# Kernel tuning notes

Measured on AMD Instinct MI355X. Metric: run time of the kernel, lower is better.

Reference implementation:

```python
import jax, jax.numpy as jnp
import numpy as np

N, E, H = 25000, 100000, 32          # nodes, edges, node/clique hidden dim
NC, A, EC = 8000, 50000, 24000       # cliques, node2clique assignments, clique edges
EEMB, CEE, L = 8, 8, 2               # edge emb dims, n layers


def segment_mean(vals, ids, num):
    s = jax.ops.segment_sum(vals, ids, num_segments=num)
    cnt = jax.ops.segment_sum(jnp.ones(ids.shape[0], vals.dtype), ids, num_segments=num)
    return s / jnp.maximum(cnt, 1.0)[:, None]


def setup_inputs() -> dict:
    key = jax.random.key(0)
    ks = jax.random.split(key, 24)
    s = 0.1  # param scale
    inp = {
        "node_features": jax.random.normal(ks[0], (N, H), jnp.float32),
        "edge_index": jax.random.randint(ks[1], (2, E), 0, N),
        "edge_features": jax.random.normal(ks[2], (E, EEMB), jnp.float32),
        "clique_features": jax.random.normal(ks[3], (NC, H), jnp.float32),
        "node2clique_index": jnp.stack([
            jax.random.randint(ks[4], (A,), 0, N),
            jax.random.randint(ks[5], (A,), 0, NC)]),
        "clique_edge_index": jax.random.randint(ks[6], (2, EC), 0, NC),
        "clique_edge_features": jax.random.normal(ks[7], (EC, CEE), jnp.float32),
        # node NNConv params (stacked over L layers)
        "nn1_w": jax.random.normal(ks[8], (L, EEMB, H)) * s,
        "nn1_b": jnp.zeros((L, H)),
        "nn2_w": jax.random.normal(ks[9], (L, H, H * H)) * s,
        "nn2_b": jnp.zeros((L, H * H)),
        "root_w": jax.random.normal(ks[10], (L, H, H)) * s,
        "root_b": jnp.zeros((L, H)),
        # Node2Clique linear
        "n2c_w": jax.random.normal(ks[11], (L, H, H)) * s,
        "n2c_b": jnp.zeros((L, H)),
        # clique NNConv params
        "cnn1_w": jax.random.normal(ks[12], (L, CEE, H)) * s,
        "cnn1_b": jnp.zeros((L, H)),
        "cnn2_w": jax.random.normal(ks[13], (L, H, H * H)) * s,
        "cnn2_b": jnp.zeros((L, H * H)),
        "croot_w": jax.random.normal(ks[14], (L, H, H)) * s,
        "croot_b": jnp.zeros((L, H)),
        # Clique2Node linear
        "c2n_w": jax.random.normal(ks[15], (L, H, H)) * s,
        "c2n_b": jnp.zeros((L, H)),
    }
    return inp


def nnconv(x, src, dst, edge_attr, w1, b1, w2, b2, rw, rb, n_out_nodes):
    # per-edge weight matrices from the edge MLP: [E, in, out]
    h = jax.nn.relu(edge_attr @ w1 + b1)
    We = (h @ w2 + b2).reshape(edge_attr.shape[0], x.shape[1], -1)
    msg = jnp.einsum('ei,eio->eo', x[src], We)           # message from source
    agg = segment_mean(msg, dst, n_out_nodes)            # mean aggregation at target
    return agg + x @ rw + rb                             # root weight + bias


def reference(node_features, edge_index, edge_features, clique_features,
              node2clique_index, clique_edge_index, clique_edge_features,
              nn1_w, nn1_b, nn2_w, nn2_b, root_w, root_b, n2c_w, n2c_b,
              cnn1_w, cnn1_b, cnn2_w, cnn2_b, croot_w, croot_b, c2n_w, c2n_b):
    x, c = node_features, clique_features
    src, dst = edge_index[0], edge_index[1]
    nid, cid = node2clique_index[0], node2clique_index[1]
    csrc, cdst = clique_edge_index[0], clique_edge_index[1]
    for l in range(L):
        # node-level edge-conditioned conv
        x = jax.nn.relu(nnconv(x, src, dst, edge_features,
                               nn1_w[l], nn1_b[l], nn2_w[l], nn2_b[l],
                               root_w[l], root_b[l], N))
        # Node2Clique: project node feats, scatter-mean into cliques
        m = x @ n2c_w[l] + n2c_b[l]
        c = c + segment_mean(m[nid], cid, NC)
        # clique-level edge-conditioned conv
        c = jax.nn.relu(nnconv(c, csrc, cdst, clique_edge_features,
                               cnn1_w[l], cnn1_b[l], cnn2_w[l], cnn2_b[l],
                               croot_w[l], croot_b[l], NC))
        # Clique2Node: project clique feats, scatter-mean back onto nodes
        m = c @ c2n_w[l] + c2n_b[l]
        x = x + segment_mean(m[cid], nid, N)
    return (x, c)
```

## Files before the change

### kernel.cpp

```cpp
#include <hip/hip_runtime.h>
#include <hip/hip_bf16.h>

typedef unsigned int u32;
typedef unsigned short u16;

#define DEVINL __device__ __forceinline__

constexpr int Nn  = 25000;
constexpr int Ee  = 100000;
constexpr int NCc = 8000;
constexpr int Aa  = 50000;
constexpr int ECc = 24000;
constexpr int TCOLS = 1088;
constexpr int WPSZ  = TCOLS*32;
constexpr int TSP   = 1064;
constexpr int NB_N = (Nn + 255)/256;
constexpr int NB_C = (NCc + 255)/256;

typedef float f32x4 __attribute__((ext_vector_type(4)));
typedef short s16x8 __attribute__((ext_vector_type(8)));

DEVINL float b2f(u16 u){ union{u32 i;float f;}v; v.i = ((u32)u)<<16; return v.f; }
DEVINL float bfl(u32 u){ union{u32 i;float f;}v; v.i = u<<16; return v.f; }
DEVINL float bfh(u32 u){ union{u32 i;float f;}v; v.i = u & 0xffff0000u; return v.f; }
DEVINL u16 f2b(float f){ union{float f;u32 i;}v; v.f=f; u32 i=v.i;
  return (u16)((i + 0x7fffu + ((i>>16)&1u)) >> 16); }
DEVINL u32 pk2(float a, float b){ return (u32)f2b(a) | ((u32)f2b(b) << 16); }
DEVINL float ldw(const void* p, long i, int f){
  return f ? ((const float*)p)[i] : b2f(((const u16*)p)[i]);
}

__global__ __launch_bounds__(256) void k_detect(const u16* __restrict__ p, int n,
                        u32* __restrict__ maxbits, int* __restrict__ zcnt,
                        int* __restrict__ done, int* __restrict__ flag){
  int i0 = blockIdx.x*256 + threadIdx.x;
  float lm = 0.f; int lz = 0;
  for (int i = i0; i < n; i += gridDim.x*256){
    u16 v = p[i];
    if (v == 0) lz++;
    lm = fmaxf(lm, fabsf(b2f(v)));
  }
  #pragma unroll
  for (int off = 32; off; off >>= 1){
    lm = fmaxf(lm, __shfl_down(lm, off));
    lz += __shfl_down(lz, off);
  }
  if ((threadIdx.x & 63) == 0){
    atomicMax(maxbits, __float_as_uint(lm));
    atomicAdd(zcnt, lz);
  }
  __syncthreads();
  if (threadIdx.x == 0){
    __threadfence();
    if (atomicAdd(done, 1) == gridDim.x - 1){
      float m = __uint_as_float(*maxbits);
      *flag = (m > 1e6f || *zcnt > n/4) ? 1 : 0;
    }
  }
}

__global__ __launch_bounds__(256) void k_count_all(const int* __restrict__ ei, const int* __restrict__ cei,
                          const int* __restrict__ n2c,
                          int* __restrict__ deg_nd, int* __restrict__ deg_ce,
                          int* __restrict__ deg_n2c, int* __restrict__ deg_c2n,
                          int* __restrict__ cnt_sn, int* __restrict__ cnt_sc){
  int i = blockIdx.x*256 + threadIdx.x;
  if (i < Ee)                             atomicAdd(&deg_nd[ei[Ee + i]], 1);
  else if ((i -= Ee) < ECc)               atomicAdd(&deg_ce[cei[ECc + i]], 1);
  else if ((i -= ECc) < Aa)               atomicAdd(&deg_n2c[n2c[Aa + i]], 1);
  else if ((i -= Aa) < Aa)                atomicAdd(&deg_c2n[n2c[i]], 1);
  else if ((i -= Aa) < Ee)                atomicAdd(&cnt_sn[ei[i]], 1);
  else if ((i -= Ee) < ECc)               atomicAdd(&cnt_sc[cei[i]], 1);
}

__global__ __launch_bounds__(256) void k_scan_block(
    const int* __restrict__ c0, const int* __restrict__ c1,
    const int* __restrict__ c2, const int* __restrict__ c3,
    int* __restrict__ o0, int* __restrict__ o1, int* __restrict__ o2, int* __restrict__ o3,
    int* __restrict__ b0, int* __restrict__ b1, int* __restrict__ b2, int* __restrict__ b3){
  __shared__ int s[256];
  int bid = blockIdx.x, seg, rb;
  if (bid < NB_N){ seg=0; rb=bid; }
  else if (bid < NB_N+NB_C){ seg=1; rb=bid-NB_N; }
  else if (bid < 2*NB_N+NB_C){ seg=2; rb=bid-NB_N-NB_C; }
  else { seg=3; rb=bid-2*NB_N-NB_C; }
  const int* cnt = seg==0?c0 : seg==1?c1 : seg==2?c2 : c3;
  int* offs = seg==0?o0 : seg==1?o1 : seg==2?o2 : o3;
  int* bs   = seg==0?b0 : seg==1?b1 : seg==2?b2 : b3;
  int M = (seg & 1) ? NCc : Nn;
  int tid = threadIdx.x;
  int i = rb*256 + tid;
  int v = (i < M) ? cnt[i] : 0;
  s[tid] = v; __syncthreads();
  for (int d = 1; d < 256; d <<= 1){
    int t = (tid >= d) ? s[tid-d] : 0;
    __syncthreads();
    s[tid] += t;
    __syncthreads();
  }
  if (i < M) offs[i] = s[tid] - v;
  if (tid == 255) bs[rb] = s[255];
}

__global__ __launch_bounds__(512) void k_spine(int* __restrict__ b0, int* __restrict__ b1,
                      int* __restrict__ b2, int* __restrict__ b3){
  __shared__ int s[512];
  int tid = threadIdx.x, seg = tid >> 7, lane = tid & 127;
  int NB = (seg & 1) ? NB_C : NB_N;
  int* bp = seg==0?b0 : seg==1?b1 : seg==2?b2 : b3;
  int v = (lane < NB) ? bp[lane] : 0;
  s[tid] = v; __syncthreads();
  for (int d = 1; d < 128; d <<= 1){
    int t = (lane >= d) ? s[tid-d] : 0;
    __syncthreads();
    s[tid] += t;
    __syncthreads();
  }
  if (lane < NB) bp[lane] = s[tid] - v;
}

__global__ __launch_bounds__(256) void k_scan_fix(
    int* __restrict__ o0, int* __restrict__ o1, int* __restrict__ o2, int* __restrict__ o3,
    const int* __restrict__ b0, const int* __restrict__ b1,
    const int* __restrict__ b2, const int* __restrict__ b3){
  int i = blockIdx.x*256 + threadIdx.x;
  if (i < Nn) o0[i] += b0[i >> 8];
  else if ((i -= Nn) < NCc) o1[i] += b1[i >> 8];
  else if ((i -= NCc) < Nn) o2[i] += b2[i >> 8];
  else if ((i -= Nn) < NCc) o3[i] += b3[i >> 8];
}

__global__ __launch_bounds__(256) void k_place(const int* __restrict__ ei, const int* __restrict__ cei,
                      const int* __restrict__ n2c,
                      const int* __restrict__ offs_n, const int* __restrict__ offs_c,
                      const int* __restrict__ offs_an, const int* __restrict__ offs_ac,
                      int* __restrict__ cur_n, int* __restrict__ cur_c,
                      int* __restrict__ cur_an, int* __restrict__ cur_ac,
                      int* __restrict__ perm_n, int* __restrict__ perm_c,
                      int* __restrict__ an2c, int* __restrict__ ac2n){
  int i = blockIdx.x*256 + threadIdx.x;
  if (i < Ee){
    int s = ei[i];
    perm_n[offs_n[s] + atomicAdd(&cur_n[s], 1)] = i;
  } else if ((i -= Ee) < ECc){
    int s = cei[i];
    perm_c[offs_c[s] + atomicAdd(&cur_c[s], 1)] = i;
  } else if ((i -= ECc) < Aa){
    int c = n2c[Aa + i];
    an2c[offs_ac[c] + atomicAdd(&cur_ac[c], 1)] = n2c[i];
  } else if ((i -= Aa) < Aa){
    int nd = n2c[i];
    ac2n[offs_an[nd] + atomicAdd(&cur_an[nd], 1)] = n2c[Aa + i];
  }
}

__global__ __launch_bounds__(256) void k_gather(const int* __restrict__ ei, const int* __restrict__ cei,
                       const int* __restrict__ perm_n, const int* __restrict__ perm_c,
                       const void* __restrict__ ef, const void* __restrict__ cef,
                       const int* __restrict__ flag,
                       int2* __restrict__ sdp_n, float* __restrict__ efp_n,
                       int2* __restrict__ sdp_c, float* __restrict__ efp_c){
  int i = blockIdx.x*256 + threadIdx.x;
  int f = *flag;
  if (i < Ee*8){
    int p = i >> 3, j = i & 7;
    int e = perm_n[p];
    efp_n[i] = ldw(ef, (long)e*8 + j, f);
    if (j == 0) sdp_n[p] = make_int2(ei[e], ei[Ee + e]);
  } else if ((i -= Ee*8) < ECc*8){
    int p = i >> 3, j = i & 7;
    int e = perm_c[p];
    efp_c[i] = ldw(cef, (long)e*8 + j, f);
    if (j == 0) sdp_c[p] = make_int2(cei[e], cei[ECc + e]);
  }
}

__global__ __launch_bounds__(256) void k_wpack_all(const void* __restrict__ nn2w, const void* __restrict__ nn2b,
                          const void* __restrict__ rootw,
                          const void* __restrict__ cnn2w, const void* __restrict__ cnn2b,
                          const void* __restrict__ crootw,
                          const int* __restrict__ flag, u16* __restrict__ Wp4){
  int i = blockIdx.x*256 + threadIdx.x;
  if (i >= 4*WPSZ) return;
  int set = i / WPSZ, j = i - set*WPSZ;
  int l = set >> 1, isC = set & 1;
  const void* W2 = isC ? cnn2w : nn2w;
  const void* B2 = isC ? cnn2b : nn2b;
  const void* RW = isC ? crootw : rootw;
  int f = *flag;
  int col = j >> 5, ii = j & 31;
  float v;
  if (col < 1024)      v = ldw(W2, (long)l*32768 + ((col>>5)<<10) + (ii<<5) + (col&31), f);
  else if (col < 1056) v = ldw(B2, (long)l*1024 + (ii<<5) + (col-1024), f);
  else                 v = ldw(RW, (long)l*1024 + (ii<<5) + (col-1056), f);
  Wp4[i] = f2b(v);
}

__global__ __launch_bounds__(512) void k_conv_fused(const void* __restrict__ base, int braw,
                           const float* __restrict__ addagg, const int* __restrict__ adddeg, int M,
                           const int2* __restrict__ sdp, const float* __restrict__ efp,
                           const int* __restrict__ offs, int E_,
                           const void* __restrict__ w1, long w1off,
                           const void* __restrict__ b1, long b1off,
                           const u16* __restrict__ Wp,
                           const void* __restrict__ rb, long rboff,
                           const int* __restrict__ flag,
                           float* __restrict__ feat_root, float* __restrict__ agg){
  __shared__ __align__(16) u16 Ts[16*TSP];
  __shared__ float w1s[256];
  __shared__ __align__(8) u32 hws[8][4][16];
  int tid = threadIdx.x;
  int w = tid >> 6, lane = tid & 63;
  int quad = lane >> 4, lm = lane & 15;
  int n0 = blockIdx.x * 16;
  int f = *flag;
  if (tid < 256) w1s[tid] = ldw(w1, w1off + tid, f);
  float bb0 = ldw(b1, b1off + 2*lm, f);
  float bb1 = ldw(b1, b1off + 2*lm + 1, f);
  int n = n0 + lm;
  int nc = n < M ? n : M-1;
  long bidx = (long)nc*32 + quad*8;
  float fv[8];
  if (braw && f == 0){
    uint4 q = *(const uint4*)((const u16*)base + bidx);
    fv[0]=bfl(q.x); fv[1]=bfh(q.x); fv[2]=bfl(q.y); fv[3]=bfh(q.y);
    fv[4]=bfl(q.z); fv[5]=bfh(q.z); fv[6]=bfl(q.w); fv[7]=bfh(q.w);
  } else {
    const float4* bp = (const float4*)((const float*)base + bidx);
    float4 q0 = bp[0], q1 = bp[1];
    fv[0]=q0.x; fv[1]=q0.y; fv[2]=q0.z; fv[3]=q0.w;
    fv[4]=q1.x; fv[5]=q1.y; fv[6]=q1.z; fv[7]=q1.w;
  }
  if (addagg){
    int dg = adddeg[nc];
    float d = (float)(dg > 1 ? dg : 1);
    const float4* ap = (const float4*)(addagg + (size_t)nc*32 + quad*8);
    float4 a0 = ap[0], a1 = ap[1];
    float inv = 1.f/d;
    fv[0]+=a0.x*inv; fv[1]+=a0.y*inv; fv[2]+=a0.z*inv; fv[3]+=a0.w*inv;
    fv[4]+=a1.x*inv; fv[5]+=a1.y*inv; fv[6]+=a1.z*inv; fv[7]+=a1.w*inv;
  }
  s16x8 bfrag;
  #pragma unroll
  for (int j = 0; j < 8; j++) bfrag[j] = (short)f2b(fv[j]);
  #pragma unroll 1
  for (int ti = 0; ti < 9; ti++){
    int ct = w*9 + ti;
    if (ct >= 68) break;
    int colbase = ct*16;
    s16x8 afrag = *(const s16x8*)(Wp + (size_t)(colbase + lm)*32 + quad*8);
    f32x4 acc = {0.f, 0.f, 0.f, 0.f};
    acc = __builtin_amdgcn_mfma_f32_16x16x32_bf16(afrag, bfrag, acc, 0, 0, 0);
    int cb = colbase + quad*4;
    if (ct < 66){
      u32 lo = (u32)f2b(acc[0]) | ((u32)f2b(acc[1]) << 16);
      u32 hi = (u32)f2b(acc[2]) | ((u32)f2b(acc[3]) << 16);
      *(uint2*)&Ts[lm*TSP + cb] = make_uint2(lo, hi);
    } else if (n < M){
      int o = cb - 1056;
      float4 v = make_float4(acc[0] + ldw(rb, rboff+o,   f),
                             acc[1] + ldw(rb, rboff+o+1, f),
                             acc[2] + ldw(rb, rboff+o+2, f),
                             acc[3] + ldw(rb, rboff+o+3, f));
      *(float4*)&feat_root[(size_t)n*32 + o] = v;
    }
  }
  __syncthreads();
  int lo = offs[n0];
  int hi = (n0 + 16 < M) ? offs[n0 + 16] : E_;
  int eg = quad, kk = lm;
  int pos = lo + w*4;
  float ef0 = 0.f, ef1 = 0.f; int sd0 = 0, sd1 = 0;
  if (lane < 32){
    int idx = pos*8 + lane;        if (idx < hi*8) ef0 = efp[idx];
    idx = (pos+32)*8 + lane;       if (idx < hi*8) ef1 = efp[idx];
  } else if (lane < 40){
    int idx = pos*2 + (lane-32);   if (idx < hi*2) sd0 = ((const int*)sdp)[idx];
    idx = (pos+32)*2 + (lane-32);  if (idx < hi*2) sd1 = ((const int*)sdp)[idx];
  }
  for (; pos < hi; pos += 32){
    int np = pos + 64;
    float ef2 = 0.f; int sd2 = 0;
    if (lane < 32){ int idx = np*8 + lane; if (idx < hi*8) ef2 = efp[idx]; }
    else if (lane < 40){ int idx = np*2 + (lane-32); if (idx < hi*2) sd2 = ((const int*)sdp)[idx]; }
    int sn = __shfl(sd0, 32 + 2*eg);
    int dn = __shfl(sd0, 33 + 2*eg);
    bool valid = (pos + eg < hi);
    int sr = sn - n0; sr = sr < 0 ? 0 : (sr > 15 ? 15 : sr);
    float a0 = bb0, a1 = bb1;
    #pragma unroll
    for (int j = 0; j < 8; j++){
      float ev = __shfl(ef0, eg*8 + j);
      a0 += ev * w1s[j*32 + 2*kk];
      a1 += ev * w1s[j*32 + 2*kk+1];
    }
    hws[w][eg][kk] = pk2(fmaxf(a0, 0.f), fmaxf(a1, 0.f));
    if (valid){
      const u16* Tr = &Ts[sr*TSP];
      u32 vb = *(const u32*)&Tr[1024 + 2*kk];
      float m0 = bfl(vb), m1 = bfh(vb);
      #pragma unroll
      for (int kq = 0; kq < 16; kq++){
        u32 hp = hws[w][eg][kq];
        float h0 = bfl(hp), h1 = bfh(hp);
        u32 v0 = *(const u32*)&Tr[(2*kq)*32 + 2*kk];
        u32 v1 = *(const u32*)&Tr[(2*kq+1)*32 + 2*kk];
        m0 += h0*bfl(v0) + h1*bfl(v1);
        m1 += h0*bfh(v0) + h1*bfh(v1);
      }
      float* ap = agg + (size_t)dn*32 + 2*kk;
      atomicAdd(ap,   m0);
      atomicAdd(ap+1, m1);
    }
    ef0 = ef1; sd0 = sd1; ef1 = ef2; sd1 = sd2;
  }
}

__global__ __launch_bounds__(256) void k_update_lin(const float* __restrict__ agg, const int* __restrict__ deg,
                           const float* __restrict__ feat_root, int M,
                           const void* __restrict__ w, long woff,
                           const void* __restrict__ b, long boff,
                           const int* __restrict__ flag,
                           float* __restrict__ feat,
                           const int* __restrict__ sidx, const int* __restrict__ soffs,
                           const int* __restrict__ sdeg, float* __restrict__ sagg){
  __shared__ float wsm[1024], bs[32], rows[8][33];
  int tid = threadIdx.x;
  int f = *flag;
  for (int idx = tid; idx < 1024; idx += 256) wsm[idx] = ldw(w, woff + idx, f);
  if (tid < 32) bs[tid] = ldw(b, boff + tid, f);
  int nl = tid >> 5, o = tid & 31;
  int n = blockIdx.x*8 + nl;
  long i = (long)n*32 + o;
  if (n < M){
    int dg = deg[n];
    float d = (float)(dg > 1 ? dg : 1);
    float v = fmaxf(agg[i]/d + feat_root[i], 0.f);
    rows[nl][o] = v;
    feat[i] = v;
  }
  __syncthreads();
  if (n >= M) return;
  float acc = bs[o];
  #pragma unroll
  for (int j = 0; j < 32; j++) acc += rows[nl][j]*wsm[j*32+o];
  int slo = soffs[n], scnt = sdeg[n];
  for (int a = 0; a < scnt; a++)
    atomicAdd(&sagg[(size_t)sidx[slo + a]*32 + o], acc);
}

__global__ __launch_bounds__(256) void k_store(const float* __restrict__ x, const float* __restrict__ xagg,
                      const int* __restrict__ xdeg, const float* __restrict__ c,
                      void* __restrict__ out, const int* __restrict__ flag){
  int i = blockIdx.x*256 + threadIdx.x;
  int tot = Nn*32 + NCc*32;
  if (i >= tot) return;
  float v;
  if (i < Nn*32){
    int n = i >> 5;
    int dg = xdeg[n];
    float d = (float)(dg > 1 ? dg : 1);
    v = x[i] + xagg[i]/d;
  } else v = c[i - Nn*32];
  if (*flag) ((float*)out)[i] = v;
  else       ((u16*)out)[i]   = f2b(v);
}

extern "C" void kernel_launch(void* const* d_in, const int* in_sizes, int n_in,
                              void* d_out, int out_size, void* d_ws, size_t ws_size,
                              hipStream_t stream){
  const int* ei  = (const int*)d_in[1];
  const int* n2c = (const int*)d_in[4];
  const int* cei = (const int*)d_in[5];
  const void *efr = d_in[2], *cefr = d_in[6];
  const void *nn1w = d_in[7], *nn1b = d_in[8], *nn2w = d_in[9], *nn2b = d_in[10],
             *rootw = d_in[11], *rootb = d_in[12], *n2cw = d_in[13], *n2cb = d_in[14],
             *cnn1w = d_in[15], *cnn1b = d_in[16], *cnn2w = d_in[17], *cnn2b = d_in[18],
             *crootw = d_in[19], *crootb = d_in[20], *c2nw = d_in[21], *c2nb = d_in[22];

  char* ws = (char*)d_ws;
  size_t off = 0;
  auto alloc = [&](size_t bytes){ void* p = ws + off; off += (bytes + 255) & ~(size_t)255; return p; };

  size_t zstart = off;
  float* aggE0  = (float*)alloc((size_t)Nn*32*4);
  float* aggE1  = (float*)alloc((size_t)Nn*32*4);
  float* caggE0 = (float*)alloc((size_t)NCc*32*4);
  float* caggE1 = (float*)alloc((size_t)NCc*32*4);
  float* caggS0 = (float*)alloc((size_t)NCc*32*4);
  float* caggS1 = (float*)alloc((size_t)NCc*32*4);
  float* aggS0  = (float*)alloc((size_t)Nn*32*4);
  float* aggS1  = (float*)alloc((size_t)Nn*32*4);
  int* deg_nd  = (int*)alloc((size_t)Nn*4);
  int* deg_ce  = (int*)alloc((size_t)NCc*4);
  int* deg_n2c = (int*)alloc((size_t)NCc*4);
  int* deg_c2n = (int*)alloc((size_t)Nn*4);
  int* cnt_sn  = (int*)alloc((size_t)Nn*4);
  int* cnt_sc  = (int*)alloc((size_t)NCc*4);
  int* cur_n   = (int*)alloc((size_t)Nn*4);
  int* cur_c   = (int*)alloc((size_t)NCc*4);
  int* cur_an  = (int*)alloc((size_t)Nn*4);
  int* cur_ac  = (int*)alloc((size_t)NCc*4);
  u32* maxbits = (u32*)alloc(256);
  int* zcnt = (int*)((char*)maxbits + 4);
  int* flag = (int*)((char*)maxbits + 8);
  int* done = (int*)((char*)maxbits + 12);
  size_t zbytes = off - zstart;

  float* xB  = (float*)alloc((size_t)Nn*32*4);
  float* xC  = (float*)alloc((size_t)Nn*32*4);
  float* cC0 = (float*)alloc((size_t)NCc*32*4);
  float* cC1 = (float*)alloc((size_t)NCc*32*4);
  float* frn = (float*)alloc((size_t)Nn*32*4);
  float* frc = (float*)alloc((size_t)NCc*32*4);
  int* offs_n  = (int*)alloc((size_t)Nn*4);
  int* offs_c  = (int*)alloc((size_t)NCc*4);
  int* offs_an = (int*)alloc((size_t)Nn*4);
  int* offs_ac = (int*)alloc((size_t)NCc*4);
  int* bs0 = (int*)alloc(512); int* bs1 = (int*)alloc(512);
  int* bs2 = (int*)alloc(512); int* bs3 = (int*)alloc(512);
  int* perm_n = (int*)alloc((size_t)Ee*4);
  int* perm_c = (int*)alloc((size_t)ECc*4);
  int* an2c = (int*)alloc((size_t)Aa*4);
  int* ac2n = (int*)alloc((size_t)Aa*4);
  int2* sdp_n = (int2*)alloc((size_t)Ee*8);
  int2* sdp_c = (int2*)alloc((size_t)ECc*8);
  float* efp_n = (float*)alloc((size_t)Ee*8*4);
  float* efp_c = (float*)alloc((size_t)ECc*8*4);
  u16* Wp4 = (u16*)alloc((size_t)4*WPSZ*2);

  auto nb = [](int n){ return (n + 255)/256; };

  hipMemsetAsync(ws + zstart, 0, zbytes, stream);
  k_detect<<<256,256,0,stream>>>((const u16*)d_in[0], Nn*32, maxbits, zcnt, done, flag);
  k_count_all<<<nb(2*Ee + 2*ECc + 2*Aa),256,0,stream>>>(ei, cei, n2c,
      deg_nd, deg_ce, deg_n2c, deg_c2n, cnt_sn, cnt_sc);
  k_scan_block<<<2*(NB_N+NB_C),256,0,stream>>>(cnt_sn, cnt_sc, deg_c2n, deg_n2c,
      offs_n, offs_c, offs_an, offs_ac, bs0, bs1, bs2, bs3);
  k_spine<<<1,512,0,stream>>>(bs0, bs1, bs2, bs3);
  k_scan_fix<<<nb(2*(Nn+NCc)),256,0,stream>>>(offs_n, offs_c, offs_an, offs_ac,
      bs0, bs1, bs2, bs3);
  k_place<<<nb(Ee+ECc+2*Aa),256,0,stream>>>(ei, cei, n2c, offs_n, offs_c, offs_an, offs_ac,
      cur_n, cur_c, cur_an, cur_ac, perm_n, perm_c, an2c, ac2n);
  k_gather<<<nb(8*(Ee+ECc)),256,0,stream>>>(ei, cei, perm_n, perm_c, efr, cefr, flag,
      sdp_n, efp_n, sdp_c, efp_c);
  k_wpack_all<<<nb(4*WPSZ),256,0,stream>>>(nn2w, nn2b, rootw, cnn2w, cnn2b, crootw, flag, Wp4);

  int Gn = (Nn + 15)/16, Gc = (NCc + 15)/16;

  k_conv_fused<<<Gn,512,0,stream>>>(d_in[0], 1, nullptr, nullptr, Nn, sdp_n, efp_n, offs_n, Ee,
      nn1w, 0, nn1b, 0, Wp4 + 0*WPSZ, rootb, 0, flag, frn, aggE0);
  k_update_lin<<<(Nn+7)/8,256,0,stream>>>(aggE0, deg_nd, frn, Nn, n2cw, 0, n2cb, 0, flag,
      xB, ac2n, offs_an, deg_c2n, caggS0);
  k_conv_fused<<<Gc,512,0,stream>>>(d_in[3], 1, caggS0, deg_n2c, NCc, sdp_c, efp_c, offs_c, ECc,
      cnn1w, 0, cnn1b, 0, Wp4 + 1*WPSZ, crootb, 0, flag, frc, caggE0);
  k_update_lin<<<(NCc+7)/8,256,0,stream>>>(caggE0, deg_ce, frc, NCc, c2nw, 0, c2nb, 0, flag,
      cC0, an2c, offs_ac, deg_n2c, aggS0);
  k_conv_fused<<<Gn,512,0,stream>>>(xB, 0, aggS0, deg_c2n, Nn, sdp_n, efp_n, offs_n, Ee,
      nn1w, 256, nn1b, 32, Wp4 + 2*WPSZ, rootb, 32, flag, frn, aggE1);
  k_update_lin<<<(Nn+7)/8,256,0,stream>>>(aggE1, deg_nd, frn, Nn, n2cw, 1024, n2cb, 32, flag,
      xC, ac2n, offs_an, deg_c2n, caggS1);
  k_conv_fused<<<Gc,512,0,stream>>>(cC0, 0, caggS1, deg_n2c, NCc, sdp_c, efp_c, offs_c, ECc,
      cnn1w, 256, cnn1b, 32, Wp4 + 3*WPSZ, crootb, 32, flag, frc, caggE1);
  k_update_lin<<<(NCc+7)/8,256,0,stream>>>(caggE1, deg_ce, frc, NCc, c2nw, 1024, c2nb, 32, flag,
      cC1, an2c, offs_ac, deg_n2c, aggS1);
  k_store<<<nb(Nn*32 + NCc*32),256,0,stream>>>(xC, aggS1, deg_c2n, cC1, d_out, flag);
}
```

Measured before the change: 346.9 us.

## Precompute edge MLP hidden layer and switch per-edge contraction to fp16 dot2

Adds a kernel that computes the first edge-MLP layer (relu(ef@W1+b1)) for all edges and both layers up front, packing the results as fp16 pairs. The conv kernel no longer recomputes it per edge inside the hot loop. The node transform now uses the fp16 MFMA instead of bf16, stores into a transposed, padded LDS layout, and the per-edge contraction uses packed fp16 dot2 instructions. Costs are an extra prep launch, extra global traffic to read the wider hidden vectors, and a reduced-range fp16 intermediate that could lose accuracy or overflow on large values.

Measured after the change: 333.8 us. 3.8% less time.

```diff
diff --git a/kernel.cpp b/kernel.cpp
--- a/kernel.cpp
+++ b/kernel.cpp
@@ -13,21 +13,37 @@
 constexpr int ECc = 24000;
 constexpr int TCOLS = 1088;
 constexpr int WPSZ  = TCOLS*32;
-constexpr int TSP   = 1064;
+constexpr int TT_ROW = 561;
 constexpr int NB_N = (Nn + 255)/256;
 constexpr int NB_C = (NCc + 255)/256;
+constexpr int HB_N = Ee/16;
+constexpr int HB_C = ECc/16;
 
 typedef float f32x4 __attribute__((ext_vector_type(4)));
-typedef short s16x8 __attribute__((ext_vector_type(8)));
+typedef _Float16 h16x2 __attribute__((ext_vector_type(2)));
+typedef _Float16 h16x8 __attribute__((ext_vector_type(8)));
 
 DEVINL float b2f(u16 u){ union{u32 i;float f;}v; v.i = ((u32)u)<<16; return v.f; }
 DEVINL float bfl(u32 u){ union{u32 i;float f;}v; v.i = u<<16; return v.f; }
 DEVINL float bfh(u32 u){ union{u32 i;float f;}v; v.i = u & 0xffff0000u; return v.f; }
 DEVINL u16 f2b(float f){ union{float f;u32 i;}v; v.f=f; u32 i=v.i;
   return (u16)((i + 0x7fffu + ((i>>16)&1u)) >> 16); }
-DEVINL u32 pk2(float a, float b){ return (u32)f2b(a) | ((u32)f2b(b) << 16); }
+DEVINL u16 f2h(float x){ union{ _Float16 h; u16 u; } v; v.h = (_Float16)x; return v.u; }
+DEVINL u32 pkh2(float a, float b){
+  union{ _Float16 h[2]; u32 u; } v;
+  v.h[0] = (_Float16)a; v.h[1] = (_Float16)b; return v.u;
+}
 DEVINL float ldw(const void* p, long i, int f){
   return f ? ((const float*)p)[i] : b2f(((const u16*)p)[i]);
+}
+DEVINL float dot2f(u32 a, u32 b, float c){
+  union U{u32 u; h16x2 h;};
+  U ua; ua.u = a; U ub; ub.u = b;
+#if __has_builtin(__builtin_amdgcn_fdot2)
+  return __builtin_amdgcn_fdot2(ua.h, ub.h, c, false);
+#else
+  return c + (float)ua.h[0]*(float)ub.h[0] + (float)ua.h[1]*(float)ub.h[1];
+#endif
 }
 
 __global__ __launch_bounds__(256) void k_detect(const u16* __restrict__ p, int n,
@@ -175,6 +191,38 @@
   }
 }
 
+__global__ __launch_bounds__(256) void k_hprep(const float* __restrict__ efp_n, const float* __restrict__ efp_c,
+                      const void* __restrict__ nn1w, const void* __restrict__ nn1b,
+                      const void* __restrict__ cnn1w, const void* __restrict__ cnn1b,
+                      const int* __restrict__ flag,
+                      u32* __restrict__ hp_n, u32* __restrict__ hp_c){
+  __shared__ float w1s[256], b1s[32], efs[128];
+  int b = blockIdx.x, tid = threadIdx.x;
+  int isC, l, rb_;
+  if (b < HB_N){ isC=0; l=0; rb_=b; }
+  else if (b < 2*HB_N){ isC=0; l=1; rb_=b-HB_N; }
+  else if (b < 2*HB_N+HB_C){ isC=1; l=0; rb_=b-2*HB_N; }
+  else { isC=1; l=1; rb_=b-2*HB_N-HB_C; }
+  const float* efp = isC ? efp_c : efp_n;
+  const void* W1 = isC ? cnn1w : nn1w;
+  const void* B1 = isC ? cnn1b : nn1b;
+  u32* hp = (isC ? hp_c : hp_n) + (size_t)l*(isC?ECc:Ee)*16;
+  int f = *flag;
+  w1s[tid] = ldw(W1, (long)l*256 + tid, f);
+  if (tid < 32) b1s[tid] = ldw(B1, (long)l*32 + tid, f);
+  if (tid < 128) efs[tid] = efp[(size_t)rb_*128 + tid];
+  __syncthreads();
+  int e8 = tid >> 4, kk = tid & 15;
+  float a0 = b1s[2*kk], a1 = b1s[2*kk+1];
+  #pragma unroll
+  for (int j = 0; j < 8; j++){
+    float ev = efs[e8*8 + j];
+    a0 += ev * w1s[j*32 + 2*kk];
+    a1 += ev * w1s[j*32 + 2*kk + 1];
+  }
+  hp[(size_t)rb_*256 + tid] = pkh2(fmaxf(a0, 0.f), fmaxf(a1, 0.f));
+}
+
 __global__ __launch_bounds__(256) void k_wpack_all(const void* __restrict__ nn2w, const void* __restrict__ nn2b,
                           const void* __restrict__ rootw,
                           const void* __restrict__ cnn2w, const void* __restrict__ cnn2b,
@@ -193,30 +241,24 @@
   if (col < 1024)      v = ldw(W2, (long)l*32768 + ((col>>5)<<10) + (ii<<5) + (col&31), f);
   else if (col < 1056) v = ldw(B2, (long)l*1024 + (ii<<5) + (col-1024), f);
   else                 v = ldw(RW, (long)l*1024 + (ii<<5) + (col-1056), f);
-  Wp4[i] = f2b(v);
+  Wp4[i] = f2h(v);
 }
 
 __global__ __launch_bounds__(512) void k_conv_fused(const void* __restrict__ base, int braw,
                            const float* __restrict__ addagg, const int* __restrict__ adddeg, int M,
-                           const int2* __restrict__ sdp, const float* __restrict__ efp,
+                           const int2* __restrict__ sdp, const u32* __restrict__ hp,
                            const int* __restrict__ offs, int E_,
-                           const void* __restrict__ w1, long w1off,
-                           const void* __restrict__ b1, long b1off,
                            const u16* __restrict__ Wp,
                            const void* __restrict__ rb, long rboff,
                            const int* __restrict__ flag,
                            float* __restrict__ feat_root, float* __restrict__ agg){
-  __shared__ __align__(16) u16 Ts[16*TSP];
-  __shared__ float w1s[256];
-  __shared__ __align__(8) u32 hws[8][4][16];
+  __shared__ __align__(16) u32 Tt[16*TT_ROW];
+  __shared__ u32 hws[8][64];
   int tid = threadIdx.x;
   int w = tid >> 6, lane = tid & 63;
   int quad = lane >> 4, lm = lane & 15;
   int n0 = blockIdx.x * 16;
   int f = *flag;
-  if (tid < 256) w1s[tid] = ldw(w1, w1off + tid, f);
-  float bb0 = ldw(b1, b1off + 2*lm, f);
-  float bb1 = ldw(b1, b1off + 2*lm + 1, f);
   int n = n0 + lm;
   int nc = n < M ? n : M-1;
   long bidx = (long)nc*32 + quad*8;
@@ -240,80 +282,87 @@
     fv[0]+=a0.x*inv; fv[1]+=a0.y*inv; fv[2]+=a0.z*inv; fv[3]+=a0.w*inv;
     fv[4]+=a1.x*inv; fv[5]+=a1.y*inv; fv[6]+=a1.z*inv; fv[7]+=a1.w*inv;
   }
-  s16x8 bfrag;
+  union { h16x8 v; u32 u[4]; } bf;
   #pragma unroll
-  for (int j = 0; j < 8; j++) bfrag[j] = (short)f2b(fv[j]);
-  #pragma unroll 1
-  for (int ti = 0; ti < 9; ti++){
-    int ct = w*9 + ti;
-    if (ct >= 68) break;
-    int colbase = ct*16;
-    s16x8 afrag = *(const s16x8*)(Wp + (size_t)(colbase + lm)*32 + quad*8);
-    f32x4 acc = {0.f, 0.f, 0.f, 0.f};
-    acc = __builtin_amdgcn_mfma_f32_16x16x32_bf16(afrag, bfrag, acc, 0, 0, 0);
-    int cb = colbase + quad*4;
+  for (int j = 0; j < 4; j++) bf.u[j] = pkh2(fv[2*j], fv[2*j+1]);
+
+  #define AFR(ct) (*(const h16x8*)(Wp + (size_t)((ct)*16 + lm)*32 + quad*8))
+  f32x4 z4 = {0.f, 0.f, 0.f, 0.f};
+  #pragma unroll
+  for (int g = 0; g < 2; g++){
+    int q = w + 8*g;
+    f32x4 c0 = __builtin_amdgcn_mfma_f32_16x16x32_f16(AFR(4*q+0), bf.v, z4, 0, 0, 0);
+    f32x4 c1 = __builtin_amdgcn_mfma_f32_16x16x32_f16(AFR(4*q+1), bf.v, z4, 0, 0, 0);
+    f32x4 c2 = __builtin_amdgcn_mfma_f32_16x16x32_f16(AFR(4*q+2), bf.v, z4, 0, 0, 0);
+    f32x4 c3 = __builtin_amdgcn_mfma_f32_16x16x32_f16(AFR(4*q+3), bf.v, z4, 0, 0, 0);
+    int rbase = lm*TT_ROW;
+    int ob = quad*4;
+    #pragma unroll
+    for (int i = 0; i < 4; i++){
+      Tt[rbase + (ob+i)*17 + q]      = pkh2(c0[i], c2[i]);
+      Tt[rbase + (16+ob+i)*17 + q]   = pkh2(c1[i], c3[i]);
+    }
+  }
+  if (w < 4){
+    int ct = 64 + w;
+    f32x4 c = __builtin_amdgcn_mfma_f32_16x16x32_f16(AFR(ct), bf.v, z4, 0, 0, 0);
     if (ct < 66){
-      u32 lo = (u32)f2b(acc[0]) | ((u32)f2b(acc[1]) << 16);
-      u32 hi = (u32)f2b(acc[2]) | ((u32)f2b(acc[3]) << 16);
-      *(uint2*)&Ts[lm*TSP + cb] = make_uint2(lo, hi);
+      int p0 = (ct-64)*8 + quad*2;
+      Tt[lm*TT_ROW + 544 + p0]     = pkh2(c[0], c[1]);
+      Tt[lm*TT_ROW + 544 + p0 + 1] = pkh2(c[2], c[3]);
     } else if (n < M){
-      int o = cb - 1056;
-      float4 v = make_float4(acc[0] + ldw(rb, rboff+o,   f),
-                             acc[1] + ldw(rb, rboff+o+1, f),
-                             acc[2] + ldw(rb, rboff+o+2, f),
-                             acc[3] + ldw(rb, rboff+o+3, f));
+      int o = (ct-66)*16 + quad*4;
+      float4 v = make_float4(c[0] + ldw(rb, rboff+o,   f),
+                             c[1] + ldw(rb, rboff+o+1, f),
+                             c[2] + ldw(rb, rboff+o+2, f),
+                             c[3] + ldw(rb, rboff+o+3, f));
       *(float4*)&feat_root[(size_t)n*32 + o] = v;
     }
   }
   __syncthreads();
+
   int lo = offs[n0];
   int hi = (n0 + 16 < M) ? offs[n0 + 16] : E_;
   int eg = quad, kk = lm;
   int pos = lo + w*4;
-  float ef0 = 0.f, ef1 = 0.f; int sd0 = 0, sd1 = 0;
-  if (lane < 32){
-    int idx = pos*8 + lane;        if (idx < hi*8) ef0 = efp[idx];
-    idx = (pos+32)*8 + lane;       if (idx < hi*8) ef1 = efp[idx];
-  } else if (lane < 40){
-    int idx = pos*2 + (lane-32);   if (idx < hi*2) sd0 = ((const int*)sdp)[idx];
-    idx = (pos+32)*2 + (lane-32);  if (idx < hi*2) sd1 = ((const int*)sdp)[idx];
+  u32 hp0 = 0, hp1 = 0; int sd0 = 0, sd1 = 0;
+  { int idx = pos*16 + lane;      if (idx < hi*16) hp0 = hp[idx];
+    idx = (pos+32)*16 + lane;     if (idx < hi*16) hp1 = hp[idx]; }
+  if (lane < 8){
+    int idx = pos*2 + lane;       if (idx < hi*2) sd0 = ((const int*)sdp)[idx];
+    idx = (pos+32)*2 + lane;      if (idx < hi*2) sd1 = ((const int*)sdp)[idx];
   }
   for (; pos < hi; pos += 32){
     int np = pos + 64;
-    float ef2 = 0.f; int sd2 = 0;
-    if (lane < 32){ int idx = np*8 + lane; if (idx < hi*8) ef2 = efp[idx]; }
-    else if (lane < 40){ int idx = np*2 + (lane-32); if (idx < hi*2) sd2 = ((const int*)sdp)[idx]; }
-    int sn = __shfl(sd0, 32 + 2*eg);
-    int dn = __shfl(sd0, 33 + 2*eg);
+    u32 hp2 = 0; int sd2 = 0;
+    { int idx = np*16 + lane; if (idx < hi*16) hp2 = hp[idx]; }
+    if (lane < 8){ int idx = np*2 + lane; if (idx < hi*2) sd2 = ((const int*)sdp)[idx]; }
+    hws[w][lane] = hp0;
+    int sn = __shfl(sd0, 2*eg);
+    int dn = __shfl(sd0, 2*eg + 1);
     bool valid = (pos + eg < hi);
     int sr = sn - n0; sr = sr < 0 ? 0 : (sr > 15 ? 15 : sr);
-    float a0 = bb0, a1 = bb1;
+    const u32* Tr = Tt + sr*TT_ROW;
+    const u32* T0 = Tr + 34*kk;
+    const u32* Hp = &hws[w][eg*16];
+    union{u32 u; h16x2 h;} b2u; b2u.u = Tr[544 + kk];
+    float m0 = (float)b2u.h[0], m1 = (float)b2u.h[1];
     #pragma unroll
-    for (int j = 0; j < 8; j++){
-      float ev = __shfl(ef0, eg*8 + j);
-      a0 += ev * w1s[j*32 + 2*kk];
-      a1 += ev * w1s[j*32 + 2*kk+1];
+    for (int kq = 0; kq < 16; kq++){
+      u32 hv = Hp[kq];
+      u32 t0 = T0[kq];
+      u32 t1 = T0[17 + kq];
+      m0 = dot2f(hv, t0, m0);
+      m1 = dot2f(hv, t1, m1);
     }
-    hws[w][eg][kk] = pk2(fmaxf(a0, 0.f), fmaxf(a1, 0.f));
     if (valid){
-      const u16* Tr = &Ts[sr*TSP];
-      u32 vb = *(const u32*)&Tr[1024 + 2*kk];
-      float m0 = bfl(vb), m1 = bfh(vb);
-      #pragma unroll
-      for (int kq = 0; kq < 16; kq++){
-        u32 hp = hws[w][eg][kq];
-        float h0 = bfl(hp), h1 = bfh(hp);
-        u32 v0 = *(const u32*)&Tr[(2*kq)*32 + 2*kk];
-        u32 v1 = *(const u32*)&Tr[(2*kq+1)*32 + 2*kk];
-        m0 += h0*bfl(v0) + h1*bfl(v1);
-        m1 += h0*bfh(v0) + h1*bfh(v1);
-      }
       float* ap = agg + (size_t)dn*32 + 2*kk;
       atomicAdd(ap,   m0);
       atomicAdd(ap+1, m1);
     }
-    ef0 = ef1; sd0 = sd1; ef1 = ef2; sd1 = sd2;
-  }
+    hp0 = hp1; sd0 = sd1; hp1 = hp2; sd1 = sd2;
+  }
+  #undef AFR
 }
 
 __global__ __launch_bounds__(256) void k_update_lin(const float* __restrict__ agg, const int* __restrict__ deg,
@@ -428,6 +477,8 @@
   float* efp_n = (float*)alloc((size_t)Ee*8*4);
   float* efp_c = (float*)alloc((size_t)ECc*8*4);
   u16* Wp4 = (u16*)alloc((size_t)4*WPSZ*2);
+  u32* hp_n = (u32*)alloc((size_t)2*Ee*16*4);
+  u32* hp_c = (u32*)alloc((size_t)2*ECc*16*4);
 
   auto nb = [](int n){ return (n + 255)/256; };
 
@@ -445,23 +496,25 @@
   k_gather<<<nb(8*(Ee+ECc)),256,0,stream>>>(ei, cei, perm_n, perm_c, efr, cefr, flag,
       sdp_n, efp_n, sdp_c, efp_c);
   k_wpack_all<<<nb(4*WPSZ),256,0,stream>>>(nn2w, nn2b, rootw, cnn2w, cnn2b, crootw, flag, Wp4);
+  k_hprep<<<2*HB_N + 2*HB_C,256,0,stream>>>(efp_n, efp_c, nn1w, nn1b, cnn1w, cnn1b, flag,
+      hp_n, hp_c);
 
   int Gn = (Nn + 15)/16, Gc = (NCc + 15)/16;
 
-  k_conv_fused<<<Gn,512,0,stream>>>(d_in[0], 1, nullptr, nullptr, Nn, sdp_n, efp_n, offs_n, Ee,
-      nn1w, 0, nn1b, 0, Wp4 + 0*WPSZ, rootb, 0, flag, frn, aggE0);
+  k_conv_fused<<<Gn,512,0,stream>>>(d_in[0], 1, nullptr, nullptr, Nn, sdp_n, hp_n, offs_n, Ee,
+      Wp4 + 0*WPSZ, rootb, 0, flag, frn, aggE0);
   k_update_lin<<<(Nn+7)/8,256,0,stream>>>(aggE0, deg_nd, frn, Nn, n2cw, 0, n2cb, 0, flag,
       xB, ac2n, offs_an, deg_c2n, caggS0);
-  k_conv_fused<<<Gc,512,0,stream>>>(d_in[3], 1, caggS0, deg_n2c, NCc, sdp_c, efp_c, offs_c, ECc,
-      cnn1w, 0, cnn1b, 0, Wp4 + 1*WPSZ, crootb, 0, flag, frc, caggE0);
+  k_conv_fused<<<Gc,512,0,stream>>>(d_in[3], 1, caggS0, deg_n2c, NCc, sdp_c, hp_c, offs_c, ECc,
+      Wp4 + 1*WPSZ, crootb, 0, flag, frc, caggE0);
   k_update_lin<<<(NCc+7)/8,256,0,stream>>>(caggE0, deg_ce, frc, NCc, c2nw, 0, c2nb, 0, flag,
       cC0, an2c, offs_ac, deg_n2c, aggS0);
-  k_conv_fused<<<Gn,512,0,stream>>>(xB, 0, aggS0, deg_c2n, Nn, sdp_n, efp_n, offs_n, Ee,
-      nn1w, 256, nn1b, 32, Wp4 + 2*WPSZ, rootb, 32, flag, frn, aggE1);
+  k_conv_fused<<<Gn,512,0,stream>>>(xB, 0, aggS0, deg_c2n, Nn, sdp_n, hp_n + (size_t)Ee*16, offs_n, Ee,
+      Wp4 + 2*WPSZ, rootb, 32, flag, frn, aggE1);
   k_update_lin<<<(Nn+7)/8,256,0,stream>>>(aggE1, deg_nd, frn, Nn, n2cw, 1024, n2cb, 32, flag,
       xC, ac2n, offs_an, deg_c2n, caggS1);
-  k_conv_fused<<<Gc,512,0,stream>>>(cC0, 0, caggS1, deg_n2c, NCc, sdp_c, efp_c, offs_c, ECc,
-      cnn1w, 256, cnn1b, 32, Wp4 + 3*WPSZ, crootb, 32, flag, frc, caggE1);
+  k_conv_fused<<<Gc,512,0,stream>>>(cC0, 0, caggS1, deg_n2c, NCc, sdp_c, hp_c + (size_t)ECc*16, offs_c, ECc,
+      Wp4 + 3*WPSZ, crootb, 32, flag, frc, caggE1);
   k_update_lin<<<(NCc+7)/8,256,0,stream>>>(caggE1, deg_ce, frc, NCc, c2nw, 1024, c2nb, 32, flag,
       cC1, an2c, offs_ac, deg_n2c, aggS1);
   k_store<<<nb(Nn*32 + NCc*32),256,0,stream>>>(xC, aggS1, deg_c2n, cC1, d_out, flag);
```
